# Performance work log

Measured on AMD Instinct MI355X. Metric: run time of the kernel, lower is better.

## Reference

```python
import jax, jax.numpy as jnp
import numpy as np

B, IN_CAPS, IN_DIM = 64, 512, 128
NUM_CAPS, DIM_CAPS, NUM_ROUTING = 32, 32, 3


def squash(x, axis=-1):
    sn = jnp.sum(x * x, axis=axis, keepdims=True)
    return (sn / (1.0 + sn)) * x / (jnp.sqrt(sn) + 1e-8)


def setup_inputs() -> dict:
    key = jax.random.key(0)
    k1, k2, k3 = jax.random.split(key, 3)
    input_tensor = jax.random.normal(k1, (B, IN_CAPS, IN_DIM), dtype=jnp.float32)
    W = 0.001 * jax.random.normal(k2, (NUM_CAPS, IN_DIM, DIM_CAPS), dtype=jnp.float32)
    b0 = jax.random.uniform(k3, (B, NUM_CAPS, IN_CAPS, 1), dtype=jnp.float32)
    return {"input_tensor": input_tensor, "W": W, "b0": b0}


def reference(input_tensor, W, b0):
    # u_hat: (B, num_caps, in_caps, dim_caps)
    u_hat = jnp.einsum('bid,ndc->bnic', input_tensor, W)
    temp_u_hat = jax.lax.stop_gradient(u_hat)
    b = b0
    for _ in range(NUM_ROUTING - 1):
        c = jax.nn.softmax(b, axis=1)            # (B, num_caps, in_caps, 1)
        s = jnp.sum(c * temp_u_hat, axis=2)      # (B, num_caps, dim_caps)
        v = squash(s)
        uv = jnp.einsum('bnic,bnc->bni', temp_u_hat, v)[..., None]
        b = b + uv
    c = jax.nn.softmax(b, axis=1)
    s = jnp.sum(c * u_hat, axis=2)
    return squash(s)                             # (B, num_caps, dim_caps)
```

## Files before the change

### kernel.cpp

```cpp
#include <hip/hip_runtime.h>
#include <math.h>

#define Bsz 64
#define IC  512
#define KD  128
#define NC  32
#define DC  32
#define CHUNK 64
#define NCH   8
#define NBLK  512
#define NTHR  256

#define CSTR 36
#define BSTR 68
#define WSTR 33

#define CXP_SZ (Bsz * NCH * NC * KD)
#define WV_SZ  (Bsz * NC * KD)

__device__ __forceinline__ int xaddr(int i, int kq) {
    return i * KD + ((((kq) + (i >> 2)) & 31) << 2);
}

__global__ __launch_bounds__(NTHR)
void kA(const float* __restrict__ bb_in, const float* __restrict__ x_g,
        const float* __restrict__ wv_g, float* __restrict__ bb_out,
        float* __restrict__ cxp, int do_uv, int write_bb)
{
    __shared__ float x_s[CHUNK * KD];
    __shared__ float bb_s[NC * BSTR];
    __shared__ float scr[KD * CSTR];

    const int t = threadIdx.x, blk = blockIdx.x;
    const int b = blk >> 3, ch = blk & 7, i0g = ch * CHUNK;

    for (int rep = 0; rep < 8; ++rep) {
        int v = t + rep * NTHR;
        int i = v >> 5, kq = v & 31;
        *(float4*)(x_s + xaddr(i, kq)) =
            *(const float4*)(x_g + ((size_t)(b * IC + i0g + i)) * KD + (kq << 2));
    }
    for (int rep = 0; rep < 2; ++rep) {
        int v = t + rep * NTHR;
        int n = v >> 4, i4 = v & 15;
        *(float4*)(bb_s + n * BSTR + (i4 << 2)) =
            *(const float4*)(bb_in + ((size_t)(b * NC + n)) * IC + i0g + (i4 << 2));
    }
    if (do_uv) {
        for (int rep = 0; rep < 4; ++rep) {
            const int n = t & 31;
            const int k4 = (t >> 5) + (rep << 3);
            float4 v4 = *(const float4*)(wv_g + ((size_t)(b * NC) + n) * KD + (k4 << 2));
            scr[(k4 * 4 + 0) * CSTR + n] = v4.x;
            scr[(k4 * 4 + 1) * CSTR + n] = v4.y;
            scr[(k4 * 4 + 2) * CSTR + n] = v4.z;
            scr[(k4 * 4 + 3) * CSTR + n] = v4.w;
        }
    }
    __syncthreads();

    if (do_uv) {
        if (t < 128) {
            const int tn = t & 7, ti = t >> 3;
            const int n0 = tn << 2, i0 = ti << 2;
            float4 a0 = {0,0,0,0}, a1 = {0,0,0,0}, a2 = {0,0,0,0}, a3 = {0,0,0,0};
            for (int kq = 0; kq < 32; ++kq) {
                const float4 xr0 = *(const float4*)(x_s + xaddr(i0 + 0, kq));
                const float4 xr1 = *(const float4*)(x_s + xaddr(i0 + 1, kq));
                const float4 xr2 = *(const float4*)(x_s + xaddr(i0 + 2, kq));
                const float4 xr3 = *(const float4*)(x_s + xaddr(i0 + 3, kq));
                const float4 w0 = *(const float4*)(scr + (kq * 4 + 0) * CSTR + n0);
                const float4 w1 = *(const float4*)(scr + (kq * 4 + 1) * CSTR + n0);
                const float4 w2 = *(const float4*)(scr + (kq * 4 + 2) * CSTR + n0);
                const float4 w3 = *(const float4*)(scr + (kq * 4 + 3) * CSTR + n0);
                a0.x += xr0.x*w0.x + xr0.y*w1.x + xr0.z*w2.x + xr0.w*w3.x;
                a0.y += xr0.x*w0.y + xr0.y*w1.y + xr0.z*w2.y + xr0.w*w3.y;
                a0.z += xr0.x*w0.z + xr0.y*w1.z + xr0.z*w2.z + xr0.w*w3.z;
                a0.w += xr0.x*w0.w + xr0.y*w1.w + xr0.z*w2.w + xr0.w*w3.w;
                a1.x += xr1.x*w0.x + xr1.y*w1.x + xr1.z*w2.x + xr1.w*w3.x;
                a1.y += xr1.x*w0.y + xr1.y*w1.y + xr1.z*w2.y + xr1.w*w3.y;
                a1.z += xr1.x*w0.z + xr1.y*w1.z + xr1.z*w2.z + xr1.w*w3.z;
                a1.w += xr1.x*w0.w + xr1.y*w1.w + xr1.z*w2.w + xr1.w*w3.w;
                a2.x += xr2.x*w0.x + xr2.y*w1.x + xr2.z*w2.x + xr2.w*w3.x;
                a2.y += xr2.x*w0.y + xr2.y*w1.y + xr2.z*w2.y + xr2.w*w3.y;
                a2.z += xr2.x*w0.z + xr2.y*w1.z + xr2.z*w2.z + xr2.w*w3.z;
                a2.w += xr2.x*w0.w + xr2.y*w1.w + xr2.z*w2.w + xr2.w*w3.w;
                a3.x += xr3.x*w0.x + xr3.y*w1.x + xr3.z*w2.x + xr3.w*w3.x;
                a3.y += xr3.x*w0.y + xr3.y*w1.y + xr3.z*w2.y + xr3.w*w3.y;
                a3.z += xr3.x*w0.z + xr3.y*w1.z + xr3.z*w2.z + xr3.w*w3.z;
                a3.w += xr3.x*w0.w + xr3.y*w1.w + xr3.z*w2.w + xr3.w*w3.w;
            }
            bb_s[(n0+0)*BSTR + i0+0] += a0.x; bb_s[(n0+1)*BSTR + i0+0] += a0.y;
            bb_s[(n0+2)*BSTR + i0+0] += a0.z; bb_s[(n0+3)*BSTR + i0+0] += a0.w;
            bb_s[(n0+0)*BSTR + i0+1] += a1.x; bb_s[(n0+1)*BSTR + i0+1] += a1.y;
            bb_s[(n0+2)*BSTR + i0+1] += a1.z; bb_s[(n0+3)*BSTR + i0+1] += a1.w;
            bb_s[(n0+0)*BSTR + i0+2] += a2.x; bb_s[(n0+1)*BSTR + i0+2] += a2.y;
            bb_s[(n0+2)*BSTR + i0+2] += a2.z; bb_s[(n0+3)*BSTR + i0+2] += a2.w;
            bb_s[(n0+0)*BSTR + i0+3] += a3.x; bb_s[(n0+1)*BSTR + i0+3] += a3.y;
            bb_s[(n0+2)*BSTR + i0+3] += a3.z; bb_s[(n0+3)*BSTR + i0+3] += a3.w;
        }
        __syncthreads();
        if (write_bb) {
            for (int rep = 0; rep < 2; ++rep) {
                int v = t + rep * NTHR;
                int n = v >> 4, i4 = v & 15;
                *(float4*)(bb_out + ((size_t)(b * NC + n)) * IC + i0g + (i4 << 2)) =
                    *(const float4*)(bb_s + n * BSTR + (i4 << 2));
            }
        }
    }

    if (t < CHUNK) {
        const int ii = t;
        float m = -1e30f;
        #pragma unroll
        for (int n = 0; n < NC; ++n) m = fmaxf(m, bb_s[n * BSTR + ii]);
        float e[NC]; float sum = 0.f;
        #pragma unroll
        for (int n = 0; n < NC; ++n) { float ev = __expf(bb_s[n * BSTR + ii] - m); e[n] = ev; sum += ev; }
        const float inv = 1.f / sum;
        float* crow = scr + ii * CSTR;
        #pragma unroll
        for (int n = 0; n < NC; ++n) crow[n] = e[n] * inv;
    }
    __syncthreads();

    {
        const int tn = t & 7, tk = t >> 3;
        const int n0 = tn << 2;
        float4 acc0 = {0,0,0,0}, acc1 = {0,0,0,0}, acc2 = {0,0,0,0}, acc3 = {0,0,0,0};
        for (int ii = 0; ii < CHUNK; ++ii) {
            const float4 c4 = *(const float4*)(scr + ii * CSTR + n0);
            const float4 x4 = *(const float4*)(x_s + xaddr(ii, tk));
            acc0.x += c4.x*x4.x; acc0.y += c4.x*x4.y; acc0.z += c4.x*x4.z; acc0.w += c4.x*x4.w;
            acc1.x += c4.y*x4.x; acc1.y += c4.y*x4.y; acc1.z += c4.y*x4.z; acc1.w += c4.y*x4.w;
            acc2.x += c4.z*x4.x; acc2.y += c4.z*x4.y; acc2.z += c4.z*x4.z; acc2.w += c4.z*x4.w;
            acc3.x += c4.w*x4.x; acc3.y += c4.w*x4.y; acc3.z += c4.w*x4.z; acc3.w += c4.w*x4.w;
        }
        float* base = cxp + ((size_t)(b * NCH + ch)) * NC * KD + (tk << 2);
        *(float4*)(base + (size_t)(n0 + 0) * KD) = acc0;
        *(float4*)(base + (size_t)(n0 + 1) * KD) = acc1;
        *(float4*)(base + (size_t)(n0 + 2) * KD) = acc2;
        *(float4*)(base + (size_t)(n0 + 3) * KD) = acc3;
    }
}

__global__ __launch_bounds__(NTHR)
void kB(const float* __restrict__ cxp, const float* __restrict__ W_g,
        float* __restrict__ wv_g, float* __restrict__ out_g, int final_)
{
    __shared__ float w_s[KD * WSTR];
    __shared__ float cxs[4 * KD];
    __shared__ float vb[4 * DC];

    const int t = threadIdx.x, blk = blockIdx.x;
    const int pb_n = blk & 31, pb_b0 = (blk >> 5) * 4;
    const int w = t >> 6, l = t & 63;
    const int b = pb_b0 + w;

    for (int rep = 0; rep < 4; ++rep) {
        int v = t + rep * NTHR;
        int k = v >> 3, d0 = (v & 7) << 2;
        float4 w4 = *(const float4*)(W_g + (size_t)pb_n * KD * DC + ((size_t)v << 2));
        float* dst = w_s + k * WSTR + d0;
        dst[0] = w4.x; dst[1] = w4.y; dst[2] = w4.z; dst[3] = w4.w;
    }
    {
        float c0 = 0.f, c1 = 0.f;
        const float* p = cxp + ((size_t)b * NCH * NC + pb_n) * KD;
        #pragma unroll
        for (int c2 = 0; c2 < NCH; ++c2) {
            c0 += p[(size_t)c2 * NC * KD + l];
            c1 += p[(size_t)c2 * NC * KD + l + 64];
        }
        cxs[w * KD + l] = c0; cxs[w * KD + l + 64] = c1;
    }
    __syncthreads();

    const int dgrp = l & 7, d0 = dgrp << 2, kg = l >> 3;
    const float* cxw = cxs + w * KD;
    float4 acc = {0,0,0,0};
    #pragma unroll
    for (int j = 0; j < 16; ++j) {
        const int k = (j << 3) + kg;
        const float* wr = w_s + k * WSTR + d0;
        const float cv = cxw[k];
        acc.x += cv * wr[0]; acc.y += cv * wr[1]; acc.z += cv * wr[2]; acc.w += cv * wr[3];
    }
    #pragma unroll
    for (int off = 8; off < 64; off <<= 1) {
        acc.x += __shfl_xor(acc.x, off, 64);
        acc.y += __shfl_xor(acc.y, off, 64);
        acc.z += __shfl_xor(acc.z, off, 64);
        acc.w += __shfl_xor(acc.w, off, 64);
    }
    float ss = acc.x*acc.x + acc.y*acc.y + acc.z*acc.z + acc.w*acc.w;
    #pragma unroll
    for (int off = 1; off < 8; off <<= 1) ss += __shfl_xor(ss, off, 64);
    const float scale = ss / ((1.f + ss) * (sqrtf(ss) + 1e-8f));
    float4 v4; v4.x = acc.x*scale; v4.y = acc.y*scale; v4.z = acc.z*scale; v4.w = acc.w*scale;

    if (final_) {
        if (kg == 0) *(float4*)(out_g + ((size_t)(b * NC) + pb_n) * DC + d0) = v4;
    } else {
        float* vbw = vb + w * DC;
        if (kg == 0) *(float4*)(vbw + d0) = v4;
        __syncthreads();
        float wv0 = 0.f, wv1 = 0.f;
        #pragma unroll
        for (int j = 0; j < 8; ++j) {
            const float4 vv = *(const float4*)(vbw + (j << 2));
            const float* wa = w_s + l * WSTR + (j << 2);
            const float* wb = w_s + (l + 64) * WSTR + (j << 2);
            wv0 += wa[0]*vv.x + wa[1]*vv.y + wa[2]*vv.z + wa[3]*vv.w;
            wv1 += wb[0]*vv.x + wb[1]*vv.y + wb[2]*vv.z + wb[3]*vv.w;
        }
        float* wrow = wv_g + ((size_t)(b * NC) + pb_n) * KD;
        wrow[l] = wv0; wrow[l + 64] = wv1;
    }
}

extern "C" void kernel_launch(void* const* d_in, const int* in_sizes, int n_in,
                              void* d_out, int out_size, void* d_ws, size_t ws_size,
                              hipStream_t stream) {
    const float* x  = (const float*)d_in[0];
    const float* W  = (const float*)d_in[1];
    const float* b0 = (const float*)d_in[2];
    float* out = (float*)d_out;

    float* cxp   = (float*)d_ws;
    float* wv    = cxp + CXP_SZ;
    float* bb_ws = wv + WV_SZ;

    kA<<<NBLK, NTHR, 0, stream>>>(b0, x, nullptr, nullptr, cxp, 0, 0);
    kB<<<NBLK, NTHR, 0, stream>>>(cxp, W, wv, nullptr, 0);
    kA<<<NBLK, NTHR, 0, stream>>>(b0, x, wv, bb_ws, cxp, 1, 1);
    kB<<<NBLK, NTHR, 0, stream>>>(cxp, W, wv, nullptr, 0);
    kA<<<NBLK, NTHR, 0, stream>>>(bb_ws, x, wv, nullptr, cxp, 1, 0);
    kB<<<NBLK, NTHR, 0, stream>>>(cxp, W, nullptr, out, 1);
}
```

Measured before the change: 128.0 us.

## Retile c·x accumulation to 8x8 register tiles with split-i shuffle reduction

The per-chunk product of softmax coefficients and x is rebuilt. Each thread now accumulates an 8-capsule by 8-dim register tile over a quarter of the input capsules, and four lanes combine their partial sums with xor shuffles. The softmax is spread over all 256 threads (four lanes per input row, shuffle-reduced max and sum) instead of only 64. The x_s swizzle is changed to match the new access pattern. The aim is fewer LDS loads per FMA and better use of the threads in the block. The cost is shuffle reduction work and more accumulator registers, and indexing the accumulator arrays with a runtime lane index may push them to scratch memory.

```diff
diff --git a/kernel.cpp b/kernel.cpp
--- a/kernel.cpp
+++ b/kernel.cpp
@@ -19,7 +19,7 @@
 #define WV_SZ  (Bsz * NC * KD)
 
 __device__ __forceinline__ int xaddr(int i, int kq) {
-    return i * KD + ((((kq) + (i >> 2)) & 31) << 2);
+    return i * KD + ((((kq) + i) & 31) << 2);
 }
 
 __global__ __launch_bounds__(NTHR)
@@ -110,38 +110,81 @@
         }
     }
 
-    if (t < CHUNK) {
-        const int ii = t;
+    {
+        const int ii = t >> 2, part = t & 3;
+        float e8[8];
         float m = -1e30f;
         #pragma unroll
-        for (int n = 0; n < NC; ++n) m = fmaxf(m, bb_s[n * BSTR + ii]);
-        float e[NC]; float sum = 0.f;
-        #pragma unroll
-        for (int n = 0; n < NC; ++n) { float ev = __expf(bb_s[n * BSTR + ii] - m); e[n] = ev; sum += ev; }
+        for (int j = 0; j < 8; ++j) {
+            e8[j] = bb_s[(part * 8 + j) * BSTR + ii];
+            m = fmaxf(m, e8[j]);
+        }
+        m = fmaxf(m, __shfl_xor(m, 1, 64));
+        m = fmaxf(m, __shfl_xor(m, 2, 64));
+        float sum = 0.f;
+        #pragma unroll
+        for (int j = 0; j < 8; ++j) { e8[j] = __expf(e8[j] - m); sum += e8[j]; }
+        sum += __shfl_xor(sum, 1, 64);
+        sum += __shfl_xor(sum, 2, 64);
         const float inv = 1.f / sum;
-        float* crow = scr + ii * CSTR;
-        #pragma unroll
-        for (int n = 0; n < NC; ++n) crow[n] = e[n] * inv;
+        float* crow = scr + ii * CSTR + part * 8;
+        #pragma unroll
+        for (int j = 0; j < 8; ++j) crow[j] = e8[j] * inv;
     }
     __syncthreads();
 
     {
-        const int tn = t & 7, tk = t >> 3;
-        const int n0 = tn << 2;
-        float4 acc0 = {0,0,0,0}, acc1 = {0,0,0,0}, acc2 = {0,0,0,0}, acc3 = {0,0,0,0};
-        for (int ii = 0; ii < CHUNK; ++ii) {
-            const float4 c4 = *(const float4*)(scr + ii * CSTR + n0);
-            const float4 x4 = *(const float4*)(x_s + xaddr(ii, tk));
-            acc0.x += c4.x*x4.x; acc0.y += c4.x*x4.y; acc0.z += c4.x*x4.z; acc0.w += c4.x*x4.w;
-            acc1.x += c4.y*x4.x; acc1.y += c4.y*x4.y; acc1.z += c4.y*x4.z; acc1.w += c4.y*x4.w;
-            acc2.x += c4.z*x4.x; acc2.y += c4.z*x4.y; acc2.z += c4.z*x4.z; acc2.w += c4.z*x4.w;
-            acc3.x += c4.w*x4.x; acc3.y += c4.w*x4.y; acc3.z += c4.w*x4.z; acc3.w += c4.w*x4.w;
-        }
-        float* base = cxp + ((size_t)(b * NCH + ch)) * NC * KD + (tk << 2);
-        *(float4*)(base + (size_t)(n0 + 0) * KD) = acc0;
-        *(float4*)(base + (size_t)(n0 + 1) * KD) = acc1;
-        *(float4*)(base + (size_t)(n0 + 2) * KD) = acc2;
-        *(float4*)(base + (size_t)(n0 + 3) * KD) = acc3;
+        const int isp = t & 3, ko = (t >> 2) & 15, no = t >> 6;
+        const int n0 = no << 3, kq0 = ko << 1;
+        float4 accA[8], accB[8];
+        #pragma unroll
+        for (int r = 0; r < 8; ++r) { accA[r] = (float4){0,0,0,0}; accB[r] = (float4){0,0,0,0}; }
+        for (int j = 0; j < 16; ++j) {
+            const int ii = (j << 2) + isp;
+            const float4 cA = *(const float4*)(scr + ii * CSTR + n0);
+            const float4 cB = *(const float4*)(scr + ii * CSTR + n0 + 4);
+            const float4 xA = *(const float4*)(x_s + xaddr(ii, kq0));
+            const float4 xB = *(const float4*)(x_s + xaddr(ii, kq0 + 1));
+            const float c0 = cA.x, c1 = cA.y, c2 = cA.z, c3 = cA.w;
+            const float c4 = cB.x, c5 = cB.y, c6 = cB.z, c7 = cB.w;
+            accA[0].x += c0*xA.x; accA[0].y += c0*xA.y; accA[0].z += c0*xA.z; accA[0].w += c0*xA.w;
+            accB[0].x += c0*xB.x; accB[0].y += c0*xB.y; accB[0].z += c0*xB.z; accB[0].w += c0*xB.w;
+            accA[1].x += c1*xA.x; accA[1].y += c1*xA.y; accA[1].z += c1*xA.z; accA[1].w += c1*xA.w;
+            accB[1].x += c1*xB.x; accB[1].y += c1*xB.y; accB[1].z += c1*xB.z; accB[1].w += c1*xB.w;
+            accA[2].x += c2*xA.x; accA[2].y += c2*xA.y; accA[2].z += c2*xA.z; accA[2].w += c2*xA.w;
+            accB[2].x += c2*xB.x; accB[2].y += c2*xB.y; accB[2].z += c2*xB.z; accB[2].w += c2*xB.w;
+            accA[3].x += c3*xA.x; accA[3].y += c3*xA.y; accA[3].z += c3*xA.z; accA[3].w += c3*xA.w;
+            accB[3].x += c3*xB.x; accB[3].y += c3*xB.y; accB[3].z += c3*xB.z; accB[3].w += c3*xB.w;
+            accA[4].x += c4*xA.x; accA[4].y += c4*xA.y; accA[4].z += c4*xA.z; accA[4].w += c4*xA.w;
+            accB[4].x += c4*xB.x; accB[4].y += c4*xB.y; accB[4].z += c4*xB.z; accB[4].w += c4*xB.w;
+            accA[5].x += c5*xA.x; accA[5].y += c5*xA.y; accA[5].z += c5*xA.z; accA[5].w += c5*xA.w;
+            accB[5].x += c5*xB.x; accB[5].y += c5*xB.y; accB[5].z += c5*xB.z; accB[5].w += c5*xB.w;
+            accA[6].x += c6*xA.x; accA[6].y += c6*xA.y; accA[6].z += c6*xA.z; accA[6].w += c6*xA.w;
+            accB[6].x += c6*xB.x; accB[6].y += c6*xB.y; accB[6].z += c6*xB.z; accB[6].w += c6*xB.w;
+            accA[7].x += c7*xA.x; accA[7].y += c7*xA.y; accA[7].z += c7*xA.z; accA[7].w += c7*xA.w;
+            accB[7].x += c7*xB.x; accB[7].y += c7*xB.y; accB[7].z += c7*xB.z; accB[7].w += c7*xB.w;
+        }
+        #pragma unroll
+        for (int r = 0; r < 8; ++r) {
+            accA[r].x += __shfl_xor(accA[r].x, 1, 64); accA[r].x += __shfl_xor(accA[r].x, 2, 64);
+            accA[r].y += __shfl_xor(accA[r].y, 1, 64); accA[r].y += __shfl_xor(accA[r].y, 2, 64);
+            accA[r].z += __shfl_xor(accA[r].z, 1, 64); accA[r].z += __shfl_xor(accA[r].z, 2, 64);
+            accA[r].w += __shfl_xor(accA[r].w, 1, 64); accA[r].w += __shfl_xor(accA[r].w, 2, 64);
+            accB[r].x += __shfl_xor(accB[r].x, 1, 64); accB[r].x += __shfl_xor(accB[r].x, 2, 64);
+            accB[r].y += __shfl_xor(accB[r].y, 1, 64); accB[r].y += __shfl_xor(accB[r].y, 2, 64);
+            accB[r].z += __shfl_xor(accB[r].z, 1, 64); accB[r].z += __shfl_xor(accB[r].z, 2, 64);
+            accB[r].w += __shfl_xor(accB[r].w, 1, 64); accB[r].w += __shfl_xor(accB[r].w, 2, 64);
+        }
+        float* base = cxp + ((size_t)(b * NCH + ch)) * NC * KD + (ko << 3);
+        {
+            const int r0 = isp, r1 = isp + 4;
+            float* p0 = base + (size_t)(n0 + r0) * KD;
+            float* p1 = base + (size_t)(n0 + r1) * KD;
+            *(float4*)(p0)     = accA[r0];
+            *(float4*)(p0 + 4) = accB[r0];
+            *(float4*)(p1)     = accA[r1];
+            *(float4*)(p1 + 4) = accB[r1];
+        }
     }
 }
 
```

Measured after the change: 150.8 us. +17.8%, slower.
